# Kernel tuning notes

Measured on AMD Instinct MI355X. Metric: run time of the kernel, lower is better.

The kernel has to match this reference:

```python
import jax, jax.numpy as jnp
import numpy as np
from jax import lax


def _conv(x, w, b):
    y = lax.conv_general_dilated(x, w, window_strides=(1, 1), padding='SAME',
                                 dimension_numbers=('NCHW', 'OIHW', 'NCHW'))
    return y + b[None, :, None, None]


def _maxpool2(x):
    return lax.reduce_window(x, -jnp.inf, lax.max,
                             window_dimensions=(1, 1, 2, 2),
                             window_strides=(1, 1, 2, 2), padding='VALID')


def setup_inputs() -> dict:
    key = jax.random.key(0)
    ks = jax.random.split(key, 11)
    f32 = jnp.float32
    return {
        'x': jax.random.normal(ks[0], (512, 1, 112, 112), f32),
        'w_conv1': jax.random.normal(ks[1], (8, 1, 3, 3), f32) * 0.1,
        'b_conv1': jax.random.normal(ks[2], (8,), f32) * 0.1,
        'w_conv2': jax.random.normal(ks[3], (16, 8, 3, 3), f32) * 0.1,
        'b_conv2': jax.random.normal(ks[4], (16,), f32) * 0.1,
        'w_patch': jax.random.normal(ks[5], (4, 64), f32) * 0.1,
        'b_patch': jax.random.normal(ks[6], (4,), f32) * 0.1,
        'w_fc1': jax.random.normal(ks[7], (64, 784), f32) * 0.05,
        'b_fc1': jax.random.normal(ks[8], (64,), f32) * 0.05,
        'w_fc2': jax.random.normal(ks[9], (10, 64), f32) * 0.05,
        'b_fc2': jax.random.normal(ks[10], (10,), f32) * 0.05,
    }


def reference(x, w_conv1, b_conv1, w_conv2, b_conv2, w_patch, b_patch,
              w_fc1, b_fc1, w_fc2, b_fc2):
    B = x.shape[0]
    h = _maxpool2(jax.nn.relu(_conv(x, w_conv1, b_conv1)))        # [B,8,56,56]
    f = _maxpool2(jax.nn.relu(_conv(h, w_conv2, b_conv2)))        # [B,16,28,28]
    C, H, W = f.shape[1], f.shape[2], f.shape[3]
    # im2col: 2x2 non-overlapping spatial patches, flattened as (C,2,2) -> 64
    p = f.reshape(B, C, H // 2, 2, W // 2, 2)
    p = p.transpose(0, 2, 4, 1, 3, 5).reshape(B, (H // 2) * (W // 2), C * 4)  # [B,196,64]
    pf = jnp.einsum('bpk,ok->bpo', p, w_patch) + b_patch          # [B,196,4]
    pf = pf.reshape(B, -1)                                        # [B,784]
    h1 = jax.nn.relu(pf @ w_fc1.T + b_fc1)
    logits = h1 @ w_fc2.T + b_fc2
    return jax.nn.log_softmax(logits, axis=-1)
```

## Files before the change

kernel.cpp:

```cpp
#include <hip/hip_runtime.h>


#define HSTR 58
#define NROWS 30
#define FSTR 33

typedef _Float16 half2_t __attribute__((ext_vector_type(2)));
typedef _Float16 f16x8 __attribute__((ext_vector_type(8)));
typedef float f32x4 __attribute__((ext_vector_type(4)));
typedef float f32x2 __attribute__((ext_vector_type(2)));

__device__ __forceinline__ unsigned pack_f16(float a, float b) {
  union { half2_t h; unsigned u; } z;
  z.h[0] = (_Float16)a;
  z.h[1] = (_Float16)b;
  return z.u;
}

__device__ __forceinline__ half2_t as_h2(unsigned u) {
  union { unsigned u; half2_t h; } z;
  z.u = u;
  return z.h;
}

__device__ __forceinline__ f16x8 as_f16x8(uint4 u) {
  union { uint4 u; f16x8 f; } z;
  z.u = u;
  return z.f;
}

__device__ __forceinline__ float fdot2_(half2_t a, half2_t b, float c) {
#if __has_builtin(__builtin_amdgcn_fdot2)
  return __builtin_amdgcn_fdot2(a, b, c, false);
#else
  return c + (float)a[0] * (float)b[0] + (float)a[1] * (float)b[1];
#endif
}

__global__ __launch_bounds__(256) void k_prew(const float* __restrict__ w2,
                                              unsigned* __restrict__ bw) {
  int t = blockIdx.x * 256 + threadIdx.x;
  if (t < 768) {
    int oc = t / 48, k32 = t % 48;
    unsigned v = 0u;
    if (k32 < 36) {
      int icp = k32 / 9, tap = k32 - icp * 9;
      v = pack_f16(w2[(oc * 8 + 2 * icp) * 9 + tap],
                   w2[(oc * 8 + 2 * icp + 1) * 9 + tap]);
    }
    bw[t] = v;
  }
}

__global__ __launch_bounds__(256, 4) void k_fused(
    const float* __restrict__ x, const float* __restrict__ w1,
    const float* __restrict__ b1, const unsigned* __restrict__ bw,
    const float* __restrict__ b2, const float* __restrict__ wp,
    const float* __restrict__ bp, const float* __restrict__ w_fc1,
    float* __restrict__ h1p) {
  __shared__ __align__(16) unsigned hsu[4 * NROWS * HSTR];
  __shared__ __align__(16) unsigned fsu[49 * FSTR];
  __shared__ __align__(16) float pfl[392];
  const int tid = threadIdx.x;
  const int b = blockIdx.x >> 1;
  const int s = blockIdx.x & 1;
  const int l = tid & 63;
  const int wv = __builtin_amdgcn_readfirstlane(tid >> 6);
  const float* xb = x + (long)b * 12544;

  unsigned wpk[32];
  {
    int ot0 = tid & 3;
#pragma unroll
    for (int i = 0; i < 32; ++i) {
      int l0 = 2 * i, l1 = 2 * i + 1;
      wpk[i] = pack_f16(wp[ot0 * 64 + (l0 & 15) * 4 + (l0 >> 4)],
                        wp[ot0 * 64 + (l1 & 15) * 4 + (l1 >> 4)]);
    }
  }
  const float bpv = bp[tid & 3];

  for (int i = tid; i < 4 * NROWS * HSTR; i += 256) hsu[i] = 0u;
  __syncthreads();

  for (int task = tid; task < 1680; task += 256) {
    int r = task / 56, hc = task % 56;
    int gr = 28 * s - 1 + r;
    if ((unsigned)gr >= 56u) continue;
    float win[4][4];
    int iy0 = 2 * gr - 1, ix0 = 2 * hc - 1;
#pragma unroll
    for (int rr = 0; rr < 4; ++rr) {
      int iy = iy0 + rr;
      bool yok = (unsigned)iy < 112u;
#pragma unroll
      for (int qq = 0; qq < 4; ++qq) {
        int ix = ix0 + qq;
        win[rr][qq] = (yok && (unsigned)ix < 112u) ? xb[iy * 112 + ix] : 0.f;
      }
    }
    float hv[8];
#pragma unroll
    for (int c = 0; c < 8; ++c) {
      f32x2 sA = {0.f, 0.f};
      f32x2 sB = {0.f, 0.f};
#pragma unroll
      for (int ty = 0; ty < 3; ++ty)
#pragma unroll
        for (int tx = 0; tx < 3; ++tx) {
          float wk = w1[c * 9 + ty * 3 + tx];
          f32x2 wkk = {wk, wk};
          f32x2 xa = {win[ty][tx], win[ty][tx + 1]};
          f32x2 xb2 = {win[ty + 1][tx], win[ty + 1][tx + 1]};
          sA = __builtin_elementwise_fma(xa, wkk, sA);
          sB = __builtin_elementwise_fma(xb2, wkk, sB);
        }
      f32x2 sm = __builtin_elementwise_max(sA, sB);
      float m = fmaxf(sm.x, sm.y);
      hv[c] = fmaxf(m + b1[c], 0.f);
    }
#pragma unroll
    for (int cp = 0; cp < 4; ++cp)
      hsu[(cp * NROWS + r) * HSTR + 1 + hc] = pack_f16(hv[2 * cp], hv[2 * cp + 1]);
  }
  __syncthreads();

  {
    const int q = l >> 4;
    int offs[12];
#pragma unroll
    for (int kk = 0; kk < 3; ++kk)
#pragma unroll
      for (int i = 0; i < 4; ++i) {
        int k32 = kk * 16 + q * 4 + i;
        int icp = k32 / 9, tap = k32 - icp * 9;
        int ty = tap / 3, tx = tap - ty * 3;
        offs[kk * 4 + i] = (icp * NROWS + ty) * HSTR + tx;
      }
    const int yoff = 2 * ((l >> 3) & 1) + ((l >> 1) & 1);
    const int xoff = 2 * ((l >> 2) & 1) + (l & 1);
    uint4 bu0 = *(const uint4*)(bw + (l & 15) * 48 + 0 * 16 + q * 4);
    uint4 bu1 = *(const uint4*)(bw + (l & 15) * 48 + 1 * 16 + q * 4);
    uint4 bu2 = *(const uint4*)(bw + (l & 15) * 48 + 2 * 16 + q * 4);
    const float b2v = b2[l & 15];
    _Float16* fsh = (_Float16*)fsu;

#pragma unroll 1
    for (int c = 0; c < 2; ++c) {
#pragma unroll 1
      for (int p_l = wv; p_l < 49; p_l += 4) {
        int p = c * 49 + p_l;
        int py = p / 14, px = p - py * 14;
        int base = (4 * py + yoff) * HSTR + 4 * px + xoff;
        uint4 a0u, a1u, a2u = make_uint4(0u, 0u, 0u, 0u);
        a0u.x = hsu[base + offs[0]];
        a0u.y = hsu[base + offs[1]];
        a0u.z = hsu[base + offs[2]];
        a0u.w = hsu[base + offs[3]];
        a1u.x = hsu[base + offs[4]];
        a1u.y = hsu[base + offs[5]];
        a1u.z = hsu[base + offs[6]];
        a1u.w = hsu[base + offs[7]];
        if (q == 0) {
          a2u.x = hsu[base + offs[8]];
          a2u.y = hsu[base + offs[9]];
          a2u.z = hsu[base + offs[10]];
          a2u.w = hsu[base + offs[11]];
        }
        f32x4 acc = {0.f, 0.f, 0.f, 0.f};
        acc = __builtin_amdgcn_mfma_f32_16x16x32_f16(as_f16x8(a0u), as_f16x8(bu0), acc, 0, 0, 0);
        acc = __builtin_amdgcn_mfma_f32_16x16x32_f16(as_f16x8(a1u), as_f16x8(bu1), acc, 0, 0, 0);
        acc = __builtin_amdgcn_mfma_f32_16x16x32_f16(as_f16x8(a2u), as_f16x8(bu2), acc, 0, 0, 0);
        float mx = fmaxf(fmaxf(acc[0], acc[1]), fmaxf(acc[2], acc[3]));
        float fv = fmaxf(mx + b2v, 0.f);
        fsh[p_l * (2 * FSTR) + l] = (_Float16)fv;
      }
      __syncthreads();
      if (tid < 196) {
        int row = tid >> 2, ot = tid & 3;
        int p = c * 49 + row;
        const unsigned* fr = fsu + row * FSTR;
        float acc = 0.f;
#pragma unroll
        for (int i = 0; i < 32; ++i) acc = fdot2_(as_h2(fr[i]), as_h2(wpk[i]), acc);
        pfl[p * 4 + ot] = acc + bpv;
      }
      __syncthreads();
    }
  }

  {
    int j = tid >> 2, q4 = tid & 3;
    const float2* wrow = (const float2*)(w_fc1 + j * 784 + 392 * s + q4 * 98);
    const float2* pv = (const float2*)(pfl + q4 * 98);
    float acc = 0.f;
#pragma unroll 7
    for (int m = 0; m < 49; ++m) {
      float2 wv2 = wrow[m], fv2 = pv[m];
      acc += wv2.x * fv2.x + wv2.y * fv2.y;
    }
    acc += __shfl_down(acc, 2, 4);
    acc += __shfl_down(acc, 1, 4);
    if (q4 == 0) h1p[((long)b * 2 + s) * 64 + j] = acc;
  }
}

__global__ __launch_bounds__(64) void k_tail(const float* __restrict__ h1p,
                                             const float* __restrict__ b_fc1,
                                             const float* __restrict__ w_fc2,
                                             const float* __restrict__ b_fc2,
                                             float* __restrict__ out) {
  __shared__ float h1s[64];
  __shared__ float red[11];
  int b = blockIdx.x, j = threadIdx.x;
  float v = b_fc1[j] + h1p[(long)b * 128 + j] + h1p[(long)b * 128 + 64 + j];
  h1s[j] = fmaxf(v, 0.f);
  __syncthreads();
  if (j < 10) {
    float acc = b_fc2[j];
    const float* wo = w_fc2 + j * 64;
#pragma unroll
    for (int k = 0; k < 64; ++k) acc += h1s[k] * wo[k];
    red[j] = acc;
  }
  __syncthreads();
  if (j == 0) {
    float mx = red[0];
    for (int o = 1; o < 10; ++o) mx = fmaxf(mx, red[o]);
    float se = 0.f;
    for (int o = 0; o < 10; ++o) se += expf(red[o] - mx);
    red[10] = mx + logf(se);
  }
  __syncthreads();
  if (j < 10) out[b * 10 + j] = red[j] - red[10];
}

extern "C" void kernel_launch(void* const* d_in, const int* in_sizes, int n_in,
                              void* d_out, int out_size, void* d_ws, size_t ws_size,
                              hipStream_t stream) {
  const float* x = (const float*)d_in[0];
  const float* w1 = (const float*)d_in[1];
  const float* b1 = (const float*)d_in[2];
  const float* w2 = (const float*)d_in[3];
  const float* b2 = (const float*)d_in[4];
  const float* wp = (const float*)d_in[5];
  const float* bp = (const float*)d_in[6];
  const float* wf1 = (const float*)d_in[7];
  const float* bf1 = (const float*)d_in[8];
  const float* wf2 = (const float*)d_in[9];
  const float* bf2 = (const float*)d_in[10];

  float* h1p = (float*)d_ws;
  unsigned* bw = (unsigned*)(h1p + 65536);

  k_prew<<<dim3(3), 256, 0, stream>>>(w2, bw);
  k_fused<<<dim3(1024), 256, 0, stream>>>(x, w1, b1, bw, b2, wp, bp, wf1, h1p);
  k_tail<<<dim3(512), 64, 0, stream>>>(h1p, bf1, wf2, bf2, (float*)d_out);
}
```

Measured before the change: 127.0 us.

## Fold weight prepack and tail kernel into fused kernel via per-sample atomic flags

Removes the separate weight-packing and tail kernels: each block now packs the conv2 MFMA B operands from w2 directly into registers, and the second block of each sample to finish (detected with an atomic counter on a per-sample flag) computes fc2 and log-softmax. A memset of the flags replaces one launch, so the chain goes from three kernel launches to a memset plus one kernel. It also unrolls the conv2 patch loop by two. The cost is redundant per-block weight loads and packing, plus threadfence and atomic overhead.

```diff
diff --git a/kernel.cpp b/kernel.cpp
--- a/kernel.cpp
+++ b/kernel.cpp
@@ -37,36 +37,45 @@
 #endif
 }
 
-__global__ __launch_bounds__(256) void k_prew(const float* __restrict__ w2,
-                                              unsigned* __restrict__ bw) {
-  int t = blockIdx.x * 256 + threadIdx.x;
-  if (t < 768) {
-    int oc = t / 48, k32 = t % 48;
-    unsigned v = 0u;
-    if (k32 < 36) {
-      int icp = k32 / 9, tap = k32 - icp * 9;
-      v = pack_f16(w2[(oc * 8 + 2 * icp) * 9 + tap],
-                   w2[(oc * 8 + 2 * icp + 1) * 9 + tap]);
-    }
-    bw[t] = v;
-  }
-}
-
 __global__ __launch_bounds__(256, 4) void k_fused(
     const float* __restrict__ x, const float* __restrict__ w1,
-    const float* __restrict__ b1, const unsigned* __restrict__ bw,
+    const float* __restrict__ b1, const float* __restrict__ w2,
     const float* __restrict__ b2, const float* __restrict__ wp,
     const float* __restrict__ bp, const float* __restrict__ w_fc1,
-    float* __restrict__ h1p) {
+    const float* __restrict__ b_fc1, const float* __restrict__ w_fc2,
+    const float* __restrict__ b_fc2, float* __restrict__ h1p,
+    int* __restrict__ flags, float* __restrict__ out) {
   __shared__ __align__(16) unsigned hsu[4 * NROWS * HSTR];
   __shared__ __align__(16) unsigned fsu[49 * FSTR];
   __shared__ __align__(16) float pfl[392];
+  __shared__ float h1s[64];
+  __shared__ float red[11];
+  __shared__ int dflag;
   const int tid = threadIdx.x;
   const int b = blockIdx.x >> 1;
   const int s = blockIdx.x & 1;
   const int l = tid & 63;
   const int wv = __builtin_amdgcn_readfirstlane(tid >> 6);
   const float* xb = x + (long)b * 12544;
+
+  const int q = l >> 4;
+  uint4 bu[3];
+#pragma unroll
+  for (int kk = 0; kk < 3; ++kk) {
+    unsigned vbits[4];
+#pragma unroll
+    for (int i = 0; i < 4; ++i) {
+      int k32 = kk * 16 + q * 4 + i;
+      unsigned v = 0u;
+      if (k32 < 36) {
+        int icp = k32 / 9, tap = k32 - icp * 9;
+        v = pack_f16(w2[((l & 15) * 8 + 2 * icp) * 9 + tap],
+                     w2[((l & 15) * 8 + 2 * icp + 1) * 9 + tap]);
+      }
+      vbits[i] = v;
+    }
+    bu[kk] = make_uint4(vbits[0], vbits[1], vbits[2], vbits[3]);
+  }
 
   unsigned wpk[32];
   {
@@ -126,7 +135,6 @@
   __syncthreads();
 
   {
-    const int q = l >> 4;
     int offs[12];
 #pragma unroll
     for (int kk = 0; kk < 3; ++kk)
@@ -139,15 +147,12 @@
       }
     const int yoff = 2 * ((l >> 3) & 1) + ((l >> 1) & 1);
     const int xoff = 2 * ((l >> 2) & 1) + (l & 1);
-    uint4 bu0 = *(const uint4*)(bw + (l & 15) * 48 + 0 * 16 + q * 4);
-    uint4 bu1 = *(const uint4*)(bw + (l & 15) * 48 + 1 * 16 + q * 4);
-    uint4 bu2 = *(const uint4*)(bw + (l & 15) * 48 + 2 * 16 + q * 4);
     const float b2v = b2[l & 15];
     _Float16* fsh = (_Float16*)fsu;
 
 #pragma unroll 1
     for (int c = 0; c < 2; ++c) {
-#pragma unroll 1
+#pragma unroll 2
       for (int p_l = wv; p_l < 49; p_l += 4) {
         int p = c * 49 + p_l;
         int py = p / 14, px = p - py * 14;
@@ -168,9 +173,9 @@
           a2u.w = hsu[base + offs[11]];
         }
         f32x4 acc = {0.f, 0.f, 0.f, 0.f};
-        acc = __builtin_amdgcn_mfma_f32_16x16x32_f16(as_f16x8(a0u), as_f16x8(bu0), acc, 0, 0, 0);
-        acc = __builtin_amdgcn_mfma_f32_16x16x32_f16(as_f16x8(a1u), as_f16x8(bu1), acc, 0, 0, 0);
-        acc = __builtin_amdgcn_mfma_f32_16x16x32_f16(as_f16x8(a2u), as_f16x8(bu2), acc, 0, 0, 0);
+        acc = __builtin_amdgcn_mfma_f32_16x16x32_f16(as_f16x8(a0u), as_f16x8(bu[0]), acc, 0, 0, 0);
+        acc = __builtin_amdgcn_mfma_f32_16x16x32_f16(as_f16x8(a1u), as_f16x8(bu[1]), acc, 0, 0, 0);
+        acc = __builtin_amdgcn_mfma_f32_16x16x32_f16(as_f16x8(a2u), as_f16x8(bu[2]), acc, 0, 0, 0);
         float mx = fmaxf(fmaxf(acc[0], acc[1]), fmaxf(acc[2], acc[3]));
         float fv = fmaxf(mx + b2v, 0.f);
         fsh[p_l * (2 * FSTR) + l] = (_Float16)fv;
@@ -203,36 +208,39 @@
     acc += __shfl_down(acc, 1, 4);
     if (q4 == 0) h1p[((long)b * 2 + s) * 64 + j] = acc;
   }
-}
-
-__global__ __launch_bounds__(64) void k_tail(const float* __restrict__ h1p,
-                                             const float* __restrict__ b_fc1,
-                                             const float* __restrict__ w_fc2,
-                                             const float* __restrict__ b_fc2,
-                                             float* __restrict__ out) {
-  __shared__ float h1s[64];
-  __shared__ float red[11];
-  int b = blockIdx.x, j = threadIdx.x;
-  float v = b_fc1[j] + h1p[(long)b * 128 + j] + h1p[(long)b * 128 + 64 + j];
-  h1s[j] = fmaxf(v, 0.f);
-  __syncthreads();
-  if (j < 10) {
-    float acc = b_fc2[j];
-    const float* wo = w_fc2 + j * 64;
-#pragma unroll
-    for (int k = 0; k < 64; ++k) acc += h1s[k] * wo[k];
-    red[j] = acc;
-  }
-  __syncthreads();
-  if (j == 0) {
-    float mx = red[0];
-    for (int o = 1; o < 10; ++o) mx = fmaxf(mx, red[o]);
-    float se = 0.f;
-    for (int o = 0; o < 10; ++o) se += expf(red[o] - mx);
-    red[10] = mx + logf(se);
-  }
-  __syncthreads();
-  if (j < 10) out[b * 10 + j] = red[j] - red[10];
+  __syncthreads();
+
+  if (tid == 0) {
+    __threadfence();
+    dflag = atomicAdd(&flags[b], 1);
+  }
+  __syncthreads();
+  if (dflag == 1) {
+    __threadfence();
+    if (tid < 64) {
+      float v = b_fc1[tid] + h1p[(long)b * 128 + tid] +
+                h1p[(long)b * 128 + 64 + tid];
+      h1s[tid] = fmaxf(v, 0.f);
+    }
+    __syncthreads();
+    if (tid < 10) {
+      float acc = b_fc2[tid];
+      const float* wo = w_fc2 + tid * 64;
+#pragma unroll
+      for (int k = 0; k < 64; ++k) acc += h1s[k] * wo[k];
+      red[tid] = acc;
+    }
+    __syncthreads();
+    if (tid == 0) {
+      float mx = red[0];
+      for (int o = 1; o < 10; ++o) mx = fmaxf(mx, red[o]);
+      float se = 0.f;
+      for (int o = 0; o < 10; ++o) se += expf(red[o] - mx);
+      red[10] = mx + logf(se);
+    }
+    __syncthreads();
+    if (tid < 10) out[b * 10 + tid] = red[tid] - red[10];
+  }
 }
 
 extern "C" void kernel_launch(void* const* d_in, const int* in_sizes, int n_in,
@@ -251,9 +259,9 @@
   const float* bf2 = (const float*)d_in[10];
 
   float* h1p = (float*)d_ws;
-  unsigned* bw = (unsigned*)(h1p + 65536);
-
-  k_prew<<<dim3(3), 256, 0, stream>>>(w2, bw);
-  k_fused<<<dim3(1024), 256, 0, stream>>>(x, w1, b1, bw, b2, wp, bp, wf1, h1p);
-  k_tail<<<dim3(512), 64, 0, stream>>>(h1p, bf1, wf2, bf2, (float*)d_out);
-}
+  int* flags = (int*)(h1p + 65536);
+
+  hipMemsetAsync(flags, 0, 512 * sizeof(int), stream);
+  k_fused<<<dim3(1024), 256, 0, stream>>>(x, w1, b1, w2, b2, wp, bp, wf1, bf1,
+                                          wf2, bf2, h1p, flags, (float*)d_out);
+}
```

Result: slower. 211.7 us (+66.7%).
